# Kernel tuning notes

Hardware: AMD Instinct MI355X
Metric: run time of the kernel (lower is better)

Reference implementation:

```python
import jax, jax.numpy as jnp
import numpy as np

BETA = 0.25  # commitment loss weight


def setup_inputs() -> dict:
    key = jax.random.key(0)
    k1, k2 = jax.random.split(key)
    z = jax.random.normal(k1, (16, 64, 32, 32), dtype=jnp.float32)      # [B,C,H,W]
    emb = jax.random.normal(k2, (8192, 64), dtype=jnp.float32)          # [V,C] codebook
    return {"z": z, "emb": emb}


def reference(z, emb):
    b, c, h, w = z.shape
    # [B,C,H,W] -> [N,C] with N = B*H*W (channels-last flatten, as in torch permute+reshape)
    z_flat = jnp.transpose(z, (0, 2, 3, 1)).reshape(-1, c)
    # squared L2 distances to every code: ||z||^2 + ||e||^2 - 2 z.e
    dist = (
        jnp.sum(z_flat * z_flat, axis=1, keepdims=True)
        + jnp.sum(emb * emb, axis=1)
        - 2.0 * (z_flat @ emb.T)
    )  # [N,V]
    idx = jnp.argmin(dist, axis=1)  # [N]
    z_q = emb[idx].reshape(b, h, w, c).transpose(0, 3, 1, 2)  # [B,C,H,W]
    codebook_loss = jnp.mean((z_q - jax.lax.stop_gradient(z)) ** 2)
    commit_loss = jnp.mean((z - jax.lax.stop_gradient(z_q)) ** 2)
    vq_loss = codebook_loss + BETA * commit_loss
    # straight-through estimator
    z_q_st = z + jax.lax.stop_gradient(z_q - z)
    return z_q_st, idx.reshape(b, h, w), vq_loss
```

## Files before the change

kernel.cpp:

```cpp
#include <hip/hip_runtime.h>


typedef _Float16 half8 __attribute__((ext_vector_type(8)));
typedef float f32x4 __attribute__((ext_vector_type(4)));

#define N_PTS 16384
#define SPLITS 4
#define THR 0.08f


__global__ __launch_bounds__(256) void k_pre(const float* __restrict__ emb,
                                             float* __restrict__ h,
                                             unsigned short* __restrict__ e16,
                                             float* __restrict__ embT,
                                             int* __restrict__ cnt) {
  int v = blockIdx.x * 256 + threadIdx.x;
  const float4* e4 = (const float4*)(emb + v * 64);
  float s = 0.f;
  float row[64];
#pragma unroll
  for (int i = 0; i < 16; ++i) {
    float4 a = e4[i];
    row[i * 4 + 0] = a.x; row[i * 4 + 1] = a.y;
    row[i * 4 + 2] = a.z; row[i * 4 + 3] = a.w;
    s += a.x * a.x + a.y * a.y + a.z * a.z + a.w * a.w;
  }
  unsigned short* base = e16 + (v >> 4) * 1024 + (v & 15) * 8;
#pragma unroll
  for (int c8 = 0; c8 < 8; ++c8) {
    half8 o;
#pragma unroll
    for (int j = 0; j < 8; ++j) o[j] = (_Float16)row[c8 * 8 + j];
    *(half8*)(base + (c8 >> 2) * 512 + (c8 & 3) * 128) = o;
  }
#pragma unroll
  for (int c = 0; c < 64; ++c) embT[c * 8192 + v] = row[c];
  h[v] = 0.5f * s;
  if (v == 0) *cnt = 0;
}

__global__ __launch_bounds__(256, 2) void k1_score(
    const float* __restrict__ z, const unsigned short* __restrict__ e16,
    const float* __restrict__ h,
    float* __restrict__ ps, float* __restrict__ pi, float* __restrict__ p2) {
  const int tid = threadIdx.x;
  const int lane = tid & 63;
  const int wid = tid >> 6;
  const int cl = lane & 15;
  const int gq = lane >> 4;
  const int n0 = blockIdx.x * 128 + wid * 32;
  const int split = blockIdx.y;

  const int b = n0 >> 10;
  const int hw0 = n0 & 1023;

  half8 A[2][2];
  {
    const float* zb = z + b * 65536 + hw0 + cl;
#pragma unroll
    for (int pt = 0; pt < 2; ++pt)
#pragma unroll
      for (int H = 0; H < 2; ++H) {
        half8 a;
#pragma unroll
        for (int j = 0; j < 8; ++j)
          a[j] = (_Float16)zb[pt * 16 + (H * 32 + gq * 8 + j) * 1024];
        A[pt][H] = a;
      }
  }

  float s1[2][4], i1f[2][4], s2[2][4];
#pragma unroll
  for (int pt = 0; pt < 2; ++pt)
#pragma unroll
    for (int r = 0; r < 4; ++r) {
      s1[pt][r] = -3.0e38f; i1f[pt][r] = 0.f; s2[pt][r] = -3.0e38f;
    }

  const int vbase = split * 2048;
  const unsigned short* bbase = e16 + (vbase >> 4) * 1024 + lane * 8;

#pragma unroll 2
  for (int T = 0; T < 128; ++T) {
    const unsigned short* bp = bbase + T * 1024;
    half8 B0 = *(const half8*)bp;
    half8 B1 = *(const half8*)(bp + 512);
    const int code = vbase + T * 16 + cl;
    const float nhv = -h[code];
    const float vf = (float)code;

#pragma unroll
    for (int pt = 0; pt < 2; ++pt) {
      f32x4 acc;
      acc[0] = nhv; acc[1] = nhv; acc[2] = nhv; acc[3] = nhv;
      acc = __builtin_amdgcn_mfma_f32_16x16x32_f16(A[pt][0], B0, acc, 0, 0, 0);
      acc = __builtin_amdgcn_mfma_f32_16x16x32_f16(A[pt][1], B1, acc, 0, 0, 0);

#pragma unroll
      for (int r = 0; r < 4; ++r) {
        float sc = acc[r];
        s2[pt][r] = fmaxf(fminf(sc, s1[pt][r]), s2[pt][r]);
        bool gt = sc > s1[pt][r];
        i1f[pt][r] = gt ? vf : i1f[pt][r];
        s1[pt][r] = fmaxf(s1[pt][r], sc);
      }
    }
  }

#pragma unroll
  for (int off = 8; off >= 1; off >>= 1) {
#pragma unroll
    for (int pt = 0; pt < 2; ++pt)
#pragma unroll
      for (int r = 0; r < 4; ++r) {
        float os = __shfl_xor(s1[pt][r], off);
        float oi = __shfl_xor(i1f[pt][r], off);
        float o2 = __shfl_xor(s2[pt][r], off);
        s2[pt][r] = fmaxf(fmaxf(s2[pt][r], o2), fminf(s1[pt][r], os));
        bool gt = os > s1[pt][r];
        i1f[pt][r] = gt ? oi : i1f[pt][r];
        s1[pt][r] = fmaxf(s1[pt][r], os);
      }
  }

  if (cl == 0) {
#pragma unroll
    for (int pt = 0; pt < 2; ++pt)
#pragma unroll
      for (int r = 0; r < 4; ++r) {
        int n = n0 + pt * 16 + gq * 4 + r;
        int o = split * N_PTS + n;
        ps[o] = s1[pt][r]; pi[o] = i1f[pt][r]; p2[o] = s2[pt][r];
      }
  }
}

__global__ __launch_bounds__(256) void k2_merge(
    const float* __restrict__ ps, const float* __restrict__ pi,
    const float* __restrict__ p2,
    int* __restrict__ idxf, float* __restrict__ out_idx,
    int* __restrict__ list, int* __restrict__ cnt) {
  int n = blockIdx.x * 256 + threadIdx.x;
  float S1 = ps[n], I1 = pi[n], S2 = p2[n];
#pragma unroll
  for (int s = 1; s < SPLITS; ++s) {
    int o = s * N_PTS + n;
    float a = ps[o], ai = pi[o], a2 = p2[o];
    if (a > S1) { S2 = fmaxf(fmaxf(S2, a2), S1); S1 = a; I1 = ai; }
    else        { S2 = fmaxf(S2, a); }
  }
  idxf[n] = (int)I1;
  out_idx[n] = I1;
  if (S1 - S2 < THR) {
    int p = atomicAdd(cnt, 1);
    list[p] = n;
  }
}

__global__ __launch_bounds__(256, 1) void k_rescue(
    const float* __restrict__ z, const float* __restrict__ embT,
    const float* __restrict__ h, const int* __restrict__ list,
    const int* __restrict__ cnt,
    int* __restrict__ idxf, float* __restrict__ out_idx) {
  __shared__ float zsT[64][4];
  __shared__ int pn[4];
  __shared__ float rs[4][4], ri[4][4];
  const int tid = threadIdx.x;
  const int lane = tid & 63, wv = tid >> 6;
  const int count = *cnt;

  for (int base = blockIdx.x * 4; base < count; base += gridDim.x * 4) {
    const int P = min(4, count - base);
    __syncthreads();
    if (tid < 4) pn[tid] = list[base + min(tid, P - 1)];
    __syncthreads();
    {
      int p = tid >> 6, c = tid & 63;
      int n = pn[p];
      zsT[c][p] = z[(n >> 10) * 65536 + c * 1024 + (n & 1023)];
    }
    __syncthreads();

    float d[128];
#pragma unroll
    for (int i = 0; i < 128; ++i) d[i] = 0.f;

    const float4* eT = (const float4*)embT;
    for (int c = 0; c < 64; ++c) {
      float4 zp = *(const float4*)&zsT[c][0];
      const float4* rowp = eT + c * 2048 + tid;
#pragma unroll
      for (int s = 0; s < 8; ++s) {
        float4 ev = rowp[s * 256];
        float* dp = d + s * 16;
        dp[0]  = fmaf(ev.x, zp.x, dp[0]);  dp[1]  = fmaf(ev.x, zp.y, dp[1]);
        dp[2]  = fmaf(ev.x, zp.z, dp[2]);  dp[3]  = fmaf(ev.x, zp.w, dp[3]);
        dp[4]  = fmaf(ev.y, zp.x, dp[4]);  dp[5]  = fmaf(ev.y, zp.y, dp[5]);
        dp[6]  = fmaf(ev.y, zp.z, dp[6]);  dp[7]  = fmaf(ev.y, zp.w, dp[7]);
        dp[8]  = fmaf(ev.z, zp.x, dp[8]);  dp[9]  = fmaf(ev.z, zp.y, dp[9]);
        dp[10] = fmaf(ev.z, zp.z, dp[10]); dp[11] = fmaf(ev.z, zp.w, dp[11]);
        dp[12] = fmaf(ev.w, zp.x, dp[12]); dp[13] = fmaf(ev.w, zp.y, dp[13]);
        dp[14] = fmaf(ev.w, zp.z, dp[14]); dp[15] = fmaf(ev.w, zp.w, dp[15]);
      }
    }

    float bs[4], bi[4];
#pragma unroll
    for (int p = 0; p < 4; ++p) { bs[p] = -3.0e38f; bi[p] = 0.f; }
#pragma unroll
    for (int s = 0; s < 8; ++s) {
      float4 hv = *(const float4*)(h + s * 1024 + tid * 4);
#pragma unroll
      for (int k = 0; k < 4; ++k) {
        float hk = (k == 0) ? hv.x : (k == 1) ? hv.y : (k == 2) ? hv.z : hv.w;
        float cf = (float)(s * 1024 + tid * 4 + k);
#pragma unroll
        for (int p = 0; p < 4; ++p) {
          float sc = d[s * 16 + k * 4 + p] - hk;
          if (sc > bs[p]) { bs[p] = sc; bi[p] = cf; }
        }
      }
    }

#pragma unroll
    for (int off = 32; off >= 1; off >>= 1) {
#pragma unroll
      for (int p = 0; p < 4; ++p) {
        float os = __shfl_xor(bs[p], off);
        float oi = __shfl_xor(bi[p], off);
        if (os > bs[p] || (os == bs[p] && oi < bi[p])) { bs[p] = os; bi[p] = oi; }
      }
    }
    if (lane == 0)
#pragma unroll
      for (int p = 0; p < 4; ++p) { rs[wv][p] = bs[p]; ri[wv][p] = bi[p]; }
    __syncthreads();
    if (tid < 4) {
      int p = tid;
      float s = rs[0][p], i = ri[0][p];
#pragma unroll
      for (int w = 1; w < 4; ++w) {
        if (rs[w][p] > s || (rs[w][p] == s && ri[w][p] < i)) { s = rs[w][p]; i = ri[w][p]; }
      }
      if (p < P) {
        int n = pn[p];
        idxf[n] = (int)i;
        out_idx[n] = i;
      }
    }
  }
}

__global__ __launch_bounds__(256) void k3_quant(
    const float* __restrict__ z, const float* __restrict__ emb,
    const int* __restrict__ idxf,
    float* __restrict__ out, float* __restrict__ psum) {
  int t = blockIdx.x * 256 + threadIdx.x;
  int g = t * 4;
  int b = g >> 16;
  int c = (g >> 10) & 63;
  int hw = g & 1023;
  int n = (b << 10) | hw;
  float4 zv = *(const float4*)(z + g);
  int4 iv = *(const int4*)(idxf + n);
  float q0 = emb[iv.x * 64 + c];
  float q1 = emb[iv.y * 64 + c];
  float q2 = emb[iv.z * 64 + c];
  float q3 = emb[iv.w * 64 + c];
  float d0 = q0 - zv.x, d1 = q1 - zv.y, d2 = q2 - zv.z, d3 = q3 - zv.w;
  float4 o;
  o.x = zv.x + d0; o.y = zv.y + d1; o.z = zv.z + d2; o.w = zv.w + d3;
  *(float4*)(out + g) = o;
  float val = d0 * d0 + d1 * d1 + d2 * d2 + d3 * d3;
#pragma unroll
  for (int off = 32; off >= 1; off >>= 1) val += __shfl_down(val, off);
  __shared__ float wsum[4];
  int lane = threadIdx.x & 63, wv = threadIdx.x >> 6;
  if (lane == 0) wsum[wv] = val;
  __syncthreads();
  if (threadIdx.x == 0)
    psum[blockIdx.x] = wsum[0] + wsum[1] + wsum[2] + wsum[3];
}

__global__ __launch_bounds__(256) void k4_loss(const float* __restrict__ psum,
                                               float* __restrict__ out_loss) {
  int tid = threadIdx.x;
  float val = psum[tid] + psum[tid + 256] + psum[tid + 512] + psum[tid + 768];
#pragma unroll
  for (int off = 32; off >= 1; off >>= 1) val += __shfl_down(val, off);
  __shared__ float wsum[4];
  int lane = tid & 63, wv = tid >> 6;
  if (lane == 0) wsum[wv] = val;
  __syncthreads();
  if (tid == 0)
    out_loss[0] = 1.25f * (wsum[0] + wsum[1] + wsum[2] + wsum[3]) * (1.0f / 1048576.0f);
}

extern "C" void kernel_launch(void* const* d_in, const int* in_sizes, int n_in,
                              void* d_out, int out_size, void* d_ws, size_t ws_size,
                              hipStream_t stream) {
  const float* z   = (const float*)d_in[0];
  const float* emb = (const float*)d_in[1];
  float* out = (float*)d_out;
  float* ws  = (float*)d_ws;

  float* h   = ws;
  unsigned short* e16 = (unsigned short*)(ws + 8192);
  float* embT = ws + 8192 + 262144;
  float* ps  = embT + 524288;
  float* pi  = ps + SPLITS * N_PTS;
  float* p2  = pi + SPLITS * N_PTS;
  int* idxf  = (int*)(p2 + SPLITS * N_PTS);
  int* list  = idxf + N_PTS;
  int* cnt   = list + N_PTS;
  float* psum = (float*)(cnt + 1);

  float* out_idx  = out + 1048576;
  float* out_loss = out + 1048576 + 16384;

  k_pre<<<32, 256, 0, stream>>>(emb, h, e16, embT, cnt);
  k1_score<<<dim3(128, SPLITS), 256, 0, stream>>>(z, e16, h, ps, pi, p2);
  k2_merge<<<64, 256, 0, stream>>>(ps, pi, p2, idxf, out_idx, list, cnt);
  k_rescue<<<512, 256, 0, stream>>>(z, embT, h, list, cnt, idxf, out_idx);
  k3_quant<<<1024, 256, 0, stream>>>(z, emb, idxf, out, psum);
  k4_loss<<<1, 256, 0, stream>>>(psum, out_loss);
}
```

Before: 158.7 us.

## Double codebook splits, raise occupancy, use fmed3, prefetch rescore embedding rows

The scoring kernel now splits the codebook into 8 chunks of 1024 codes instead of 4 of 2048, and its launch bound asks for 4 blocks per CU instead of 2, giving more parallel blocks and shorter loops. The second-best tracking uses a single fmed3 instead of a min/max pair. The fp32 rescore loop software-prefetches the next channel's embedding row into registers while computing the current one, to hide global load latency. The risks are higher register pressure from the prefetch buffer and the tighter launch bound, possibly causing spills, plus more partial results to merge downstream.

```diff
diff --git a/kernel.cpp b/kernel.cpp
--- a/kernel.cpp
+++ b/kernel.cpp
@@ -5,7 +5,7 @@
 typedef float f32x4 __attribute__((ext_vector_type(4)));
 
 #define N_PTS 16384
-#define SPLITS 4
+#define SPLITS 8
 #define THR 0.08f
 
 
@@ -39,7 +39,7 @@
   if (v == 0) *cnt = 0;
 }
 
-__global__ __launch_bounds__(256, 2) void k1_score(
+__global__ __launch_bounds__(256, 4) void k1_score(
     const float* __restrict__ z, const unsigned short* __restrict__ e16,
     const float* __restrict__ h,
     float* __restrict__ ps, float* __restrict__ pi, float* __restrict__ p2) {
@@ -77,11 +77,11 @@
       s1[pt][r] = -3.0e38f; i1f[pt][r] = 0.f; s2[pt][r] = -3.0e38f;
     }
 
-  const int vbase = split * 2048;
-  const unsigned short* bbase = e16 + (vbase >> 4) * 1024 + lane * 8;
+  const int vbase = split * 1024;
+  const unsigned short* bbase = e16 + vbase * 64 + lane * 8;
 
 #pragma unroll 2
-  for (int T = 0; T < 128; ++T) {
+  for (int T = 0; T < 64; ++T) {
     const unsigned short* bp = bbase + T * 1024;
     half8 B0 = *(const half8*)bp;
     half8 B1 = *(const half8*)(bp + 512);
@@ -99,7 +99,7 @@
 #pragma unroll
       for (int r = 0; r < 4; ++r) {
         float sc = acc[r];
-        s2[pt][r] = fmaxf(fminf(sc, s1[pt][r]), s2[pt][r]);
+        s2[pt][r] = __builtin_amdgcn_fmed3f(sc, s1[pt][r], s2[pt][r]);
         bool gt = sc > s1[pt][r];
         i1f[pt][r] = gt ? vf : i1f[pt][r];
         s1[pt][r] = fmaxf(s1[pt][r], sc);
@@ -186,12 +186,40 @@
     for (int i = 0; i < 128; ++i) d[i] = 0.f;
 
     const float4* eT = (const float4*)embT;
-    for (int c = 0; c < 64; ++c) {
+
+    float4 cur[8];
+#pragma unroll
+    for (int s = 0; s < 8; ++s) cur[s] = eT[s * 256 + tid];
+
+#pragma unroll 2
+    for (int c = 0; c < 63; ++c) {
+      float4 nxt[8];
+      const float4* rowp = eT + (c + 1) * 2048 + tid;
+#pragma unroll
+      for (int s = 0; s < 8; ++s) nxt[s] = rowp[s * 256];
+
       float4 zp = *(const float4*)&zsT[c][0];
-      const float4* rowp = eT + c * 2048 + tid;
 #pragma unroll
       for (int s = 0; s < 8; ++s) {
-        float4 ev = rowp[s * 256];
+        float4 ev = cur[s];
+        float* dp = d + s * 16;
+        dp[0]  = fmaf(ev.x, zp.x, dp[0]);  dp[1]  = fmaf(ev.x, zp.y, dp[1]);
+        dp[2]  = fmaf(ev.x, zp.z, dp[2]);  dp[3]  = fmaf(ev.x, zp.w, dp[3]);
+        dp[4]  = fmaf(ev.y, zp.x, dp[4]);  dp[5]  = fmaf(ev.y, zp.y, dp[5]);
+        dp[6]  = fmaf(ev.y, zp.z, dp[6]);  dp[7]  = fmaf(ev.y, zp.w, dp[7]);
+        dp[8]  = fmaf(ev.z, zp.x, dp[8]);  dp[9]  = fmaf(ev.z, zp.y, dp[9]);
+        dp[10] = fmaf(ev.z, zp.z, dp[10]); dp[11] = fmaf(ev.z, zp.w, dp[11]);
+        dp[12] = fmaf(ev.w, zp.x, dp[12]); dp[13] = fmaf(ev.w, zp.y, dp[13]);
+        dp[14] = fmaf(ev.w, zp.z, dp[14]); dp[15] = fmaf(ev.w, zp.w, dp[15]);
+      }
+#pragma unroll
+      for (int s = 0; s < 8; ++s) cur[s] = nxt[s];
+    }
+    {
+      float4 zp = *(const float4*)&zsT[63][0];
+#pragma unroll
+      for (int s = 0; s < 8; ++s) {
+        float4 ev = cur[s];
         float* dp = d + s * 16;
         dp[0]  = fmaf(ev.x, zp.x, dp[0]);  dp[1]  = fmaf(ev.x, zp.y, dp[1]);
         dp[2]  = fmaf(ev.x, zp.z, dp[2]);  dp[3]  = fmaf(ev.x, zp.w, dp[3]);
```

Result: faster. 154.9 us (-2.4%).

## Double codebook splits in scoring and widen rescue kernel to 1024 threads

Applied to the files above, without the earlier changes.

The scoring kernel now splits the codebook into 8 chunks instead of 4 and requests 4 blocks per SIMD group. This gives more blocks, more parallelism and higher occupancy, at the cost of more partial results for the merge kernel to combine. The top-2 update uses a single fmed3 instruction. The rescue kernel runs 1024-thread blocks with 8 codes per thread instead of 32, which cuts register pressure, and it prefetches the next channel's embedding values. The reduction across 16 waves grows to match.

```diff
diff --git a/kernel.cpp b/kernel.cpp
--- a/kernel.cpp
+++ b/kernel.cpp
@@ -5,7 +5,7 @@
 typedef float f32x4 __attribute__((ext_vector_type(4)));
 
 #define N_PTS 16384
-#define SPLITS 4
+#define SPLITS 8
 #define THR 0.08f
 
 
@@ -39,7 +39,7 @@
   if (v == 0) *cnt = 0;
 }
 
-__global__ __launch_bounds__(256, 2) void k1_score(
+__global__ __launch_bounds__(256, 4) void k1_score(
     const float* __restrict__ z, const unsigned short* __restrict__ e16,
     const float* __restrict__ h,
     float* __restrict__ ps, float* __restrict__ pi, float* __restrict__ p2) {
@@ -77,11 +77,11 @@
       s1[pt][r] = -3.0e38f; i1f[pt][r] = 0.f; s2[pt][r] = -3.0e38f;
     }
 
-  const int vbase = split * 2048;
-  const unsigned short* bbase = e16 + (vbase >> 4) * 1024 + lane * 8;
+  const int vbase = split * 1024;
+  const unsigned short* bbase = e16 + vbase * 64 + lane * 8;
 
 #pragma unroll 2
-  for (int T = 0; T < 128; ++T) {
+  for (int T = 0; T < 64; ++T) {
     const unsigned short* bp = bbase + T * 1024;
     half8 B0 = *(const half8*)bp;
     half8 B1 = *(const half8*)(bp + 512);
@@ -99,7 +99,7 @@
 #pragma unroll
       for (int r = 0; r < 4; ++r) {
         float sc = acc[r];
-        s2[pt][r] = fmaxf(fminf(sc, s1[pt][r]), s2[pt][r]);
+        s2[pt][r] = __builtin_amdgcn_fmed3f(sc, s1[pt][r], s2[pt][r]);
         bool gt = sc > s1[pt][r];
         i1f[pt][r] = gt ? vf : i1f[pt][r];
         s1[pt][r] = fmaxf(s1[pt][r], sc);
@@ -157,14 +157,14 @@
   }
 }
 
-__global__ __launch_bounds__(256, 1) void k_rescue(
+__global__ __launch_bounds__(1024, 4) void k_rescue(
     const float* __restrict__ z, const float* __restrict__ embT,
     const float* __restrict__ h, const int* __restrict__ list,
     const int* __restrict__ cnt,
     int* __restrict__ idxf, float* __restrict__ out_idx) {
   __shared__ float zsT[64][4];
   __shared__ int pn[4];
-  __shared__ float rs[4][4], ri[4][4];
+  __shared__ float rs[16][4], ri[16][4];
   const int tid = threadIdx.x;
   const int lane = tid & 63, wv = tid >> 6;
   const int count = *cnt;
@@ -174,51 +174,56 @@
     __syncthreads();
     if (tid < 4) pn[tid] = list[base + min(tid, P - 1)];
     __syncthreads();
-    {
+    if (tid < 256) {
       int p = tid >> 6, c = tid & 63;
       int n = pn[p];
       zsT[c][p] = z[(n >> 10) * 65536 + c * 1024 + (n & 1023)];
     }
     __syncthreads();
 
-    float d[128];
-#pragma unroll
-    for (int i = 0; i < 128; ++i) d[i] = 0.f;
+    float d[32];
+#pragma unroll
+    for (int i = 0; i < 32; ++i) d[i] = 0.f;
 
     const float4* eT = (const float4*)embT;
+    float4 cur0 = eT[tid];
+    float4 cur1 = eT[1024 + tid];
+
     for (int c = 0; c < 64; ++c) {
+      float4 nxt0, nxt1;
+      if (c < 63) {
+        const float4* rowp = eT + (c + 1) * 2048 + tid;
+        nxt0 = rowp[0];
+        nxt1 = rowp[1024];
+      }
       float4 zp = *(const float4*)&zsT[c][0];
-      const float4* rowp = eT + c * 2048 + tid;
-#pragma unroll
-      for (int s = 0; s < 8; ++s) {
-        float4 ev = rowp[s * 256];
-        float* dp = d + s * 16;
-        dp[0]  = fmaf(ev.x, zp.x, dp[0]);  dp[1]  = fmaf(ev.x, zp.y, dp[1]);
-        dp[2]  = fmaf(ev.x, zp.z, dp[2]);  dp[3]  = fmaf(ev.x, zp.w, dp[3]);
-        dp[4]  = fmaf(ev.y, zp.x, dp[4]);  dp[5]  = fmaf(ev.y, zp.y, dp[5]);
-        dp[6]  = fmaf(ev.y, zp.z, dp[6]);  dp[7]  = fmaf(ev.y, zp.w, dp[7]);
-        dp[8]  = fmaf(ev.z, zp.x, dp[8]);  dp[9]  = fmaf(ev.z, zp.y, dp[9]);
-        dp[10] = fmaf(ev.z, zp.z, dp[10]); dp[11] = fmaf(ev.z, zp.w, dp[11]);
-        dp[12] = fmaf(ev.w, zp.x, dp[12]); dp[13] = fmaf(ev.w, zp.y, dp[13]);
-        dp[14] = fmaf(ev.w, zp.z, dp[14]); dp[15] = fmaf(ev.w, zp.w, dp[15]);
-      }
-    }
-
+      float ev[8] = {cur0.x, cur0.y, cur0.z, cur0.w,
+                     cur1.x, cur1.y, cur1.z, cur1.w};
+#pragma unroll
+      for (int k = 0; k < 8; ++k) {
+        d[k * 4 + 0] = fmaf(ev[k], zp.x, d[k * 4 + 0]);
+        d[k * 4 + 1] = fmaf(ev[k], zp.y, d[k * 4 + 1]);
+        d[k * 4 + 2] = fmaf(ev[k], zp.z, d[k * 4 + 2]);
+        d[k * 4 + 3] = fmaf(ev[k], zp.w, d[k * 4 + 3]);
+      }
+      if (c < 63) { cur0 = nxt0; cur1 = nxt1; }
+    }
+
+    float4 hv0 = *(const float4*)(h + tid * 4);
+    float4 hv1 = *(const float4*)(h + 4096 + tid * 4);
     float bs[4], bi[4];
 #pragma unroll
     for (int p = 0; p < 4; ++p) { bs[p] = -3.0e38f; bi[p] = 0.f; }
 #pragma unroll
-    for (int s = 0; s < 8; ++s) {
-      float4 hv = *(const float4*)(h + s * 1024 + tid * 4);
-#pragma unroll
-      for (int k = 0; k < 4; ++k) {
-        float hk = (k == 0) ? hv.x : (k == 1) ? hv.y : (k == 2) ? hv.z : hv.w;
-        float cf = (float)(s * 1024 + tid * 4 + k);
-#pragma unroll
-        for (int p = 0; p < 4; ++p) {
-          float sc = d[s * 16 + k * 4 + p] - hk;
-          if (sc > bs[p]) { bs[p] = sc; bi[p] = cf; }
-        }
+    for (int k = 0; k < 8; ++k) {
+      float hk = (k == 0) ? hv0.x : (k == 1) ? hv0.y : (k == 2) ? hv0.z :
+                 (k == 3) ? hv0.w : (k == 4) ? hv1.x : (k == 5) ? hv1.y :
+                 (k == 6) ? hv1.z : hv1.w;
+      float cf = (float)((k < 4 ? 0 : 4096) + tid * 4 + (k & 3));
+#pragma unroll
+      for (int p = 0; p < 4; ++p) {
+        float sc = d[k * 4 + p] - hk;
+        if (sc > bs[p]) { bs[p] = sc; bi[p] = cf; }
       }
     }
 
@@ -239,7 +244,7 @@
       int p = tid;
       float s = rs[0][p], i = ri[0][p];
 #pragma unroll
-      for (int w = 1; w < 4; ++w) {
+      for (int w = 1; w < 16; ++w) {
         if (rs[w][p] > s || (rs[w][p] == s && ri[w][p] < i)) { s = rs[w][p]; i = ri[w][p]; }
       }
       if (p < P) {
@@ -321,7 +326,7 @@
   k_pre<<<32, 256, 0, stream>>>(emb, h, e16, embT, cnt);
   k1_score<<<dim3(128, SPLITS), 256, 0, stream>>>(z, e16, h, ps, pi, p2);
   k2_merge<<<64, 256, 0, stream>>>(ps, pi, p2, idxf, out_idx, list, cnt);
-  k_rescue<<<512, 256, 0, stream>>>(z, embT, h, list, cnt, idxf, out_idx);
+  k_rescue<<<256, 1024, 0, stream>>>(z, embT, h, list, cnt, idxf, out_idx);
   k3_quant<<<1024, 256, 0, stream>>>(z, emb, idxf, out, psum);
   k4_loss<<<1, 256, 0, stream>>>(psum, out_loss);
 }
```

After: 145.2 us. -8.5%, faster.
